# Kernel optimization log

Measured on AMD Instinct MI355X. Metric: run time of the kernel, lower is better.

## Reference

```python
import jax, jax.numpy as jnp
import numpy as np

TOP_K = 8
ALPHA = 0.1
EPS = 1e-20


def setup_inputs() -> dict:
    key = jax.random.key(0)
    k1, k2 = jax.random.split(key)
    B, S, D, E = 4, 8192, 1024, 64
    hidden_states = jax.random.normal(k1, (B, S, D), dtype=jnp.float32)
    # kaiming_uniform_(a=sqrt(5)) on [E, D] -> bound = 1/sqrt(D)
    bound = 1.0 / np.sqrt(D)
    W = jax.random.uniform(k2, (E, D), dtype=jnp.float32, minval=-bound, maxval=bound)
    return {"hidden_states": hidden_states, "W": W}


def reference(hidden_states, W):
    B, S, D = hidden_states.shape
    E = W.shape[0]
    x = hidden_states.reshape(-1, D)                       # [T, D], T = B*S
    logits = jnp.einsum('td,ed->te', x, W)                 # [T, E]
    scores = jax.nn.softmax(logits, axis=-1)               # [T, E]
    top_k_weights, top_k_idx = jax.lax.top_k(scores, TOP_K)  # [T, K]
    # norm_topk_experts renormalization
    top_k_weights = top_k_weights / (top_k_weights.sum(axis=-1, keepdims=True) + EPS)
    # seq_aux loss: per-batch expert selection counts via scatter-add
    idx = top_k_idx.reshape(B, -1)                         # [B, S*K]
    ce = jnp.zeros((B, E), dtype=jnp.float32).at[jnp.arange(B)[:, None], idx].add(1.0)
    mean_scores = scores.reshape(B, S, E).mean(axis=1)     # [B, E]
    aux_loss = (ce * mean_scores).sum(axis=1).mean() * ALPHA
    return top_k_idx, top_k_weights, aux_loss
```

## Files before the change

### kernel.cpp

```cpp
#include <hip/hip_runtime.h>

#define TOKS   32768
#define NEXP   64
#define DDIM   1024
#define SEQ    8192
#define NBATCH 4
#define TPB    64
#define STR    68
#define CSTR   21
#define BK     128
#define NCHK   (DDIM / BK)

typedef __attribute__((ext_vector_type(8)))  short short8v;
typedef __attribute__((ext_vector_type(16))) float f32x16;

__device__ __forceinline__ unsigned f2bf(float x) {
  unsigned u = __float_as_uint(x);
  return (u + 0x7fffu + ((u >> 16) & 1u)) >> 16;
}
__device__ __forceinline__ float bf2f(unsigned h) { return __uint_as_float(h << 16); }

__global__ void moe_wsplit(const float* __restrict__ W, ushort* __restrict__ W3) {
  const int sid = blockIdx.x * 256 + threadIdx.x;
  const int p  = sid & 3;
  const int e  = (sid >> 2) & 63;
  const int g  = sid >> 8;
  const int kh = p & 1;
  const int k0 = g * 16 + kh * 8;
  const float* src = W + (size_t)e * DDIM + k0;
  float f[8];
  *(float4*)&f[0] = *(const float4*)src;
  *(float4*)&f[4] = *(const float4*)(src + 4);
  ushort o[8];
  if (p < 2) {
#pragma unroll
    for (int j = 0; j < 8; ++j) o[j] = (ushort)f2bf(f[j]);
  } else {
#pragma unroll
    for (int j = 0; j < 8; ++j) {
      unsigned hb = f2bf(f[j]);
      o[j] = (ushort)f2bf(f[j] - bf2f(hb));
    }
  }
  *(short8v*)(W3 + (size_t)sid * 8) = *(const short8v*)o;
}

__global__ __launch_bounds__(256, 3) void moe_gate_main(
    const float* __restrict__ X, const ushort* __restrict__ W3,
    float* __restrict__ out, float* __restrict__ gsum, float* __restrict__ gce,
    int* __restrict__ flag_cnt, int* __restrict__ flag_tok)
{
  __shared__ __align__(16) char smem[47104];

  float* xs   = (float*)smem;
  float* wsm  = (float*)(smem + 17408);
  float* red  = (float*)(smem + 34816);
  float* gmx  = (float*)(smem + 35840);
  float* cval = (float*)(smem + 36096);
  int*   cidx = (int*)  (smem + 41472);
  int*   hist = (int*)  (smem + 46848);

  const int tid = threadIdx.x;
  const int tok_base = blockIdx.x * TPB;
  const int bb = blockIdx.x >> 7;

  const int l = tid & 63, q = tid >> 6;
  const int wm = q >> 1, wn = q & 1;
  const int rr = l & 31;
  const int kh = l >> 5;

  const int xr0 = tid >> 5;
  const int xc  = tid & 31;
  const float* Xbase = X + (size_t)tok_base * DDIM;
  int wb[8];
#pragma unroll
  for (int i = 0; i < 8; ++i) {
    const int r = xr0 + 8 * i;
    wb[i] = r * 256 + ((((xc >> 1) ^ (r & 15)) << 4)) + ((xc & 1) * 8);
  }

  const int abase = (wm * 32 + rr) * 256;
  const int amask = (wm * 32 + rr) & 15;
  const ushort* Wb = W3 + (size_t)(wn * 32 + rr) * 32 + kh * 8;

  f32x16 accA = (f32x16)0.0f, accB = (f32x16)0.0f;

  float4 px[8];
  unsigned sh[16], sl[16];

#define LOADPX(kc) do { \
    const float* xsrc = Xbase + (kc) * BK; \
    _Pragma("unroll") \
    for (int i = 0; i < 8; ++i) \
      px[i] = *(const float4*)(xsrc + (size_t)(xr0 + 8 * i) * DDIM + xc * 4); \
  } while (0)

#define CONV() do { \
    _Pragma("unroll") \
    for (int i = 0; i < 8; ++i) { \
      unsigned h0 = f2bf(px[i].x), h1 = f2bf(px[i].y); \
      unsigned h2 = f2bf(px[i].z), h3 = f2bf(px[i].w); \
      sh[2 * i]     = h0 | (h1 << 16); \
      sh[2 * i + 1] = h2 | (h3 << 16); \
      sl[2 * i]     = f2bf(px[i].x - bf2f(h0)) | (f2bf(px[i].y - bf2f(h1)) << 16); \
      sl[2 * i + 1] = f2bf(px[i].z - bf2f(h2)) | (f2bf(px[i].w - bf2f(h3)) << 16); \
    } } while (0)

#define WRITE() do { \
    _Pragma("unroll") \
    for (int i = 0; i < 8; ++i) { \
      *(uint2*)(smem + wb[i])         = make_uint2(sh[2 * i], sh[2 * i + 1]); \
      *(uint2*)(smem + 16384 + wb[i]) = make_uint2(sl[2 * i], sl[2 * i + 1]); \
    } } while (0)

#define COMPUTE(kc) do { \
    _Pragma("unroll") \
    for (int s = 0; s < 8; ++s) { \
      const int g = (kc) * 8 + s; \
      const ushort* wp = Wb + (size_t)g * 2048; \
      short8v bh = *(const short8v*)wp; \
      short8v bl = *(const short8v*)(wp + 16); \
      const int aoff = abase + (((2 * s + kh) ^ amask) << 4); \
      short8v ah = *(const short8v*)(smem + aoff); \
      short8v al = *(const short8v*)(smem + 16384 + aoff); \
      accA = __builtin_amdgcn_mfma_f32_32x32x16_bf16(ah, bh, accA, 0, 0, 0); \
      accB = __builtin_amdgcn_mfma_f32_32x32x16_bf16(al, bh, accB, 0, 0, 0); \
      accA = __builtin_amdgcn_mfma_f32_32x32x16_bf16(ah, bl, accA, 0, 0, 0); \
    } } while (0)

  LOADPX(0);
  CONV();
  WRITE();
  __syncthreads();

#pragma unroll 1
  for (int kc = 0; kc < NCHK; ++kc) {
    if (kc + 1 < NCHK) LOADPX(kc + 1);
    COMPUTE(kc);
    if (kc + 1 < NCHK) CONV();
    __syncthreads();
    if (kc + 1 < NCHK) {
      WRITE();
      __syncthreads();
    }
  }

  {
    const int ccol = wn * 32 + rr;
#pragma unroll
    for (int r = 0; r < 16; ++r) {
      const int trow = wm * 32 + (r & 3) + 8 * (r >> 2) + 4 * kh;
      wsm[trow * STR + ccol] = accA[r] + accB[r];
    }
  }
  if (tid < 64) hist[tid] = 0;
  __syncthreads();

#undef LOADPX
#undef CONV
#undef WRITE
#undef COMPUTE

  float* logits  = wsm;
  float* scoresT = xs;
  const int t = l;

  float m = -__builtin_huge_valf();
#pragma unroll
  for (int e = 0; e < 16; ++e) m = fmaxf(m, logits[t * STR + q * 16 + e]);
  red[q * 64 + t] = m;
  __syncthreads();
  float gm = fmaxf(fmaxf(red[t], red[64 + t]), fmaxf(red[128 + t], red[192 + t]));
  if (q == 0) gmx[t] = gm;
  float z = 0.0f;
#pragma unroll
  for (int e = 0; e < 16; ++e) {
    float ev = expf(logits[t * STR + q * 16 + e] - gm);
    scoresT[(q * 16 + e) * STR + t] = ev;
    z += ev;
  }
  __syncthreads();
  red[q * 64 + t] = z;
  __syncthreads();
  float Z = red[t] + red[64 + t] + red[128 + t] + red[192 + t];
  float invZ = 1.0f / Z;
#pragma unroll
  for (int e = 0; e < 16; ++e) scoresT[(q * 16 + e) * STR + t] *= invZ;
  __syncthreads();

  {
    const int e = l, g = q;
    float s = 0.0f;
#pragma unroll
    for (int tt = 0; tt < 16; ++tt) s += scoresT[e * STR + g * 16 + tt];
    red[g * 64 + e] = s;
  }
  __syncthreads();
  if (tid < 64) {
    float tot = red[tid] + red[64 + tid] + red[128 + tid] + red[192 + tid];
    atomicAdd(&gsum[bb * 64 + tid], tot);
  }

  if (tid < 128) {
    const int h = tid >> 6;
    const int eb = h * 32;
#pragma unroll 1
    for (int k = 0; k < 9; ++k) {
      float mv = -1.0f; int mi = eb;
#pragma unroll 4
      for (int e = 0; e < 32; ++e) {
        float v = scoresT[(eb + e) * STR + t];
        if (v > mv) { mv = v; mi = eb + e; }
      }
      cval[t * CSTR + h * 9 + k] = mv;
      cidx[t * CSTR + h * 9 + k] = mi;
      scoresT[mi * STR + t] = -1.0f;
    }
  }
  __syncthreads();

  if (tid < 64) {
    float wv[9]; int wi[8];
#pragma unroll 1
    for (int k = 0; k < 9; ++k) {
      float mv = -1.0f; int mj = 0;
#pragma unroll 3
      for (int j = 0; j < 18; ++j) {
        float v = cval[t * CSTR + j];
        if (v > mv) { mv = v; mj = j; }
      }
      wv[k] = mv;
      if (k < 8) {
        wi[k] = cidx[t * CSTR + mj];
        atomicAdd(&hist[wi[k]], 1);
      }
      cval[t * CSTR + mj] = -1.0f;
    }
    bool flag = false;
#pragma unroll
    for (int k = 0; k < 8; ++k)
      if (wv[k + 1] >= wv[k] * (1.0f - 2.0e-5f)) flag = true;
    if (flag) {
      int p = atomicAdd(flag_cnt, 1);
      flag_tok[p] = tok_base + t;
    }
    double ed[8]; double den = 0.0;
#pragma unroll
    for (int k = 0; k < 8; ++k) {
      ed[k] = exp((double)logits[t * STR + wi[k]] - (double)gmx[t]);
      den += ed[k];
    }
    const size_t tg = (size_t)(tok_base + t);
    *(float4*)(out + tg * 8) =
        make_float4((float)wi[0], (float)wi[1], (float)wi[2], (float)wi[3]);
    *(float4*)(out + tg * 8 + 4) =
        make_float4((float)wi[4], (float)wi[5], (float)wi[6], (float)wi[7]);
    *(float4*)(out + (size_t)TOKS * 8 + tg * 8) =
        make_float4((float)(ed[0] / den), (float)(ed[1] / den),
                    (float)(ed[2] / den), (float)(ed[3] / den));
    *(float4*)(out + (size_t)TOKS * 8 + tg * 8 + 4) =
        make_float4((float)(ed[4] / den), (float)(ed[5] / den),
                    (float)(ed[6] / den), (float)(ed[7] / den));
  }
  __syncthreads();
  if (tid < 64) atomicAdd(&gce[bb * 64 + tid], (float)hist[tid]);
}

__global__ __launch_bounds__(256) void moe_refine(
    const float* __restrict__ X, const float* __restrict__ W,
    float* __restrict__ out, float* __restrict__ gce,
    const int* __restrict__ flag_cnt, const int* __restrict__ flag_tok)
{
  __shared__ __align__(16) float xrow[DDIM];
  __shared__ double part[4][NEXP];
  const int tid = threadIdx.x;
  const int n = *flag_cnt;
  const int e = tid & 63;
  const int c = tid >> 6;
#pragma unroll 1
  for (int it = blockIdx.x; it < n; it += 256) {
    const int tok = flag_tok[it];
    __syncthreads();
    *(float4*)&xrow[tid * 4] = *(const float4*)&X[(size_t)tok * DDIM + tid * 4];
    __syncthreads();
    const float* wr = W + (size_t)e * DDIM + c * 256;
    const float* xr = xrow + c * 256;
    double s0 = 0.0, s1 = 0.0, s2 = 0.0, s3 = 0.0;
#pragma unroll 4
    for (int j = 0; j < 256; j += 4) {
      s0 += (double)xr[j]     * (double)wr[j];
      s1 += (double)xr[j + 1] * (double)wr[j + 1];
      s2 += (double)xr[j + 2] * (double)wr[j + 2];
      s3 += (double)xr[j + 3] * (double)wr[j + 3];
    }
    part[c][e] = (s0 + s1) + (s2 + s3);
    __syncthreads();
    if (tid < 64) {
      double cur = (part[0][e] + part[1][e]) + (part[2][e] + part[3][e]);
      int wi[8]; double wl[8];
#pragma unroll 1
      for (int k = 0; k < 8; ++k) {
        double mv = cur; int mi = e;
#pragma unroll
        for (int off = 1; off < 64; off <<= 1) {
          double ov = __shfl_xor(mv, off);
          int    oi = __shfl_xor(mi, off);
          if (ov > mv || (ov == mv && oi < mi)) { mv = ov; mi = oi; }
        }
        wi[k] = mi; wl[k] = mv;
        if (e == mi) cur = -1.0e300;
      }
      if (e == 0) {
        int olde[8];
#pragma unroll
        for (int k = 0; k < 8; ++k) olde[k] = (int)out[(size_t)tok * 8 + k];
        double ex[8]; double den = 0.0;
#pragma unroll
        for (int k = 0; k < 8; ++k) { ex[k] = exp(wl[k] - wl[0]); den += ex[k]; }
#pragma unroll
        for (int k = 0; k < 8; ++k) {
          out[(size_t)tok * 8 + k] = (float)wi[k];
          out[(size_t)TOKS * 8 + (size_t)tok * 8 + k] = (float)(ex[k] / den);
        }
        const int bbb = tok >> 13;
#pragma unroll 1
        for (int k = 0; k < 8; ++k) {
          bool in_new = false, in_old = false;
          for (int j = 0; j < 8; ++j) {
            if (wi[j] == olde[k]) in_new = true;
            if (olde[j] == wi[k]) in_old = true;
          }
          if (!in_new) atomicAdd(&gce[bbb * 64 + olde[k]], -1.0f);
          if (!in_old) atomicAdd(&gce[bbb * 64 + wi[k]], 1.0f);
        }
      }
    }
  }
}

__global__ void moe_gate_aux(const float* __restrict__ gsum,
                             const float* __restrict__ gce,
                             float* __restrict__ out)
{
  __shared__ float r[256];
  const int tid = threadIdx.x;
  r[tid] = gce[tid] * gsum[tid];
  __syncthreads();
  for (int s = 128; s > 0; s >>= 1) {
    if (tid < s) r[tid] += r[tid + s];
    __syncthreads();
  }
  if (tid == 0)
    out[(size_t)TOKS * 16] = 0.1f * r[0] / ((float)SEQ * (float)NBATCH);
}

extern "C" void kernel_launch(void* const* d_in, const int* in_sizes, int n_in,
                              void* d_out, int out_size, void* d_ws, size_t ws_size,
                              hipStream_t stream)
{
  const float* X = (const float*)d_in[0];
  const float* W = (const float*)d_in[1];
  float* out  = (float*)d_out;
  float* gsum = (float*)d_ws;
  float* gce  = gsum + NBATCH * NEXP;
  int* flag_cnt = (int*)((char*)d_ws + 2048);
  int* flag_tok = (int*)((char*)d_ws + 2176);
  ushort* W3 = (ushort*)((char*)d_ws + (1 << 20));

  hipMemsetAsync(d_ws, 0, 2176, stream);
  moe_wsplit<<<64, 256, 0, stream>>>(W, W3);
  moe_gate_main<<<TOKS / TPB, 256, 0, stream>>>(X, W3, out, gsum, gce, flag_cnt, flag_tok);
  moe_refine<<<256, 256, 0, stream>>>(X, W, out, gce, flag_cnt, flag_tok);
  moe_gate_aux<<<1, 256, 0, stream>>>(gsum, gce, out);
}
```

Baseline: 254.9 us.

## Split gate GEMM into separate small-tile kernel with double-buffered LDS

The fused GEMM and softmax/top-k kernel is split in two. A new GEMM kernel handles 16 tokens per block with 16x16x32 MFMAs, a double-buffered LDS tile, and one __syncthreads per K chunk, and it writes fp32 logits to workspace. A separate epilogue kernel reads those logits back and does softmax/top-k. The aim is more blocks, higher occupancy and better latency hiding for the memory-bound X stream, paid for with an extra logits round trip through global memory and one more launch.

```diff
diff --git a/kernel.cpp b/kernel.cpp
--- a/kernel.cpp
+++ b/kernel.cpp
@@ -8,11 +8,9 @@
 #define TPB    64
 #define STR    68
 #define CSTR   21
-#define BK     128
-#define NCHK   (DDIM / BK)
 
 typedef __attribute__((ext_vector_type(8)))  short short8v;
-typedef __attribute__((ext_vector_type(16))) float f32x16;
+typedef __attribute__((ext_vector_type(4)))  float f32x4;
 
 __device__ __forceinline__ unsigned f2bf(float x) {
   unsigned u = __float_as_uint(x);
@@ -20,19 +18,21 @@
 }
 __device__ __forceinline__ float bf2f(unsigned h) { return __uint_as_float(h << 16); }
 
-__global__ void moe_wsplit(const float* __restrict__ W, ushort* __restrict__ W3) {
+__global__ void moe_wsplit(const float* __restrict__ W, ushort* __restrict__ W4) {
   const int sid = blockIdx.x * 256 + threadIdx.x;
-  const int p  = sid & 3;
-  const int e  = (sid >> 2) & 63;
-  const int g  = sid >> 8;
-  const int kh = p & 1;
-  const int k0 = g * 16 + kh * 8;
+  const int table = sid >> 13;
+  const int s2 = sid & 8191;
+  const int g  = s2 >> 8;
+  const int r  = s2 & 255;
+  const int e  = r >> 2;
+  const int kh = r & 3;
+  const int k0 = g * 32 + kh * 8;
   const float* src = W + (size_t)e * DDIM + k0;
   float f[8];
   *(float4*)&f[0] = *(const float4*)src;
   *(float4*)&f[4] = *(const float4*)(src + 4);
   ushort o[8];
-  if (p < 2) {
+  if (table == 0) {
 #pragma unroll
     for (int j = 0; j < 8; ++j) o[j] = (ushort)f2bf(f[j]);
   } else {
@@ -42,11 +42,97 @@
       o[j] = (ushort)f2bf(f[j] - bf2f(hb));
     }
   }
-  *(short8v*)(W3 + (size_t)sid * 8) = *(const short8v*)o;
-}
-
-__global__ __launch_bounds__(256, 3) void moe_gate_main(
-    const float* __restrict__ X, const ushort* __restrict__ W3,
+  *(short8v*)(W4 + (size_t)sid * 8) = *(const short8v*)o;
+}
+
+__global__ __launch_bounds__(256, 6) void moe_gemm(
+    const float* __restrict__ X, const ushort* __restrict__ W4,
+    float* __restrict__ Lg)
+{
+  __shared__ __align__(16) char smem[16384];
+
+  const int tid = threadIdx.x;
+  const int l = tid & 63, w = tid >> 6;
+  const int tok_base = blockIdx.x * 16;
+
+  const int sr = tid >> 4;
+  const int sp = tid & 15;
+  const float* Xr = X + (size_t)(tok_base + sr) * DDIM + sp * 8;
+  const int wofs = sr * 256 + ((sp ^ sr) << 4);
+
+  const int kg = l >> 4;
+  const int abase = (l & 15) * 256;
+  const int axor = l & 15;
+  const char* Wb = (const char*)W4 + w * 1024 + (l & 15) * 64 + kg * 16;
+
+  f32x4 acc = (f32x4)0.0f;
+  float4 px0, px1;
+  unsigned vh[4], vl[4];
+
+#define LOADPX(kc) do { \
+    px0 = *(const float4*)(Xr + (kc) * 128); \
+    px1 = *(const float4*)(Xr + (kc) * 128 + 4); } while (0)
+
+#define CONV() do { \
+    float ff[8] = {px0.x, px0.y, px0.z, px0.w, px1.x, px1.y, px1.z, px1.w}; \
+    _Pragma("unroll") \
+    for (int i = 0; i < 4; ++i) { \
+      unsigned h0 = f2bf(ff[2 * i]), h1 = f2bf(ff[2 * i + 1]); \
+      vh[i] = h0 | (h1 << 16); \
+      vl[i] = f2bf(ff[2 * i] - bf2f(h0)) | (f2bf(ff[2 * i + 1] - bf2f(h1)) << 16); \
+    } } while (0)
+
+#define WRITE(b) do { \
+    *(uint4*)(smem + (b) * 8192 + wofs)        = make_uint4(vh[0], vh[1], vh[2], vh[3]); \
+    *(uint4*)(smem + (b) * 8192 + 4096 + wofs) = make_uint4(vl[0], vl[1], vl[2], vl[3]); \
+    } while (0)
+
+#define COMPUTE(kc) do { \
+    const char* base = smem + ((kc) & 1) * 8192; \
+    _Pragma("unroll") \
+    for (int s = 0; s < 4; ++s) { \
+      const char* wp = Wb + (size_t)((kc) * 4 + s) * 4096; \
+      short8v bh = *(const short8v*)wp; \
+      short8v bl = *(const short8v*)(wp + 131072); \
+      const int aoff = abase + (((4 * s + kg) ^ axor) << 4); \
+      short8v ah = *(const short8v*)(base + aoff); \
+      short8v al = *(const short8v*)(base + aoff + 4096); \
+      acc = __builtin_amdgcn_mfma_f32_16x16x32_bf16(ah, bh, acc, 0, 0, 0); \
+      acc = __builtin_amdgcn_mfma_f32_16x16x32_bf16(al, bh, acc, 0, 0, 0); \
+      acc = __builtin_amdgcn_mfma_f32_16x16x32_bf16(ah, bl, acc, 0, 0, 0); \
+    } } while (0)
+
+  LOADPX(0);
+  CONV();
+  WRITE(0);
+  LOADPX(1);
+  __syncthreads();
+
+#pragma unroll 1
+  for (int kc = 0; kc < 8; ++kc) {
+    if (kc + 1 < 8) {
+      CONV();
+      WRITE((kc + 1) & 1);
+    }
+    if (kc + 2 < 8) LOADPX(kc + 2);
+    COMPUTE(kc);
+    __syncthreads();
+  }
+
+#undef LOADPX
+#undef CONV
+#undef WRITE
+#undef COMPUTE
+
+  {
+    float* dst = Lg + (size_t)(tok_base + kg * 4) * NEXP + w * 16 + (l & 15);
+#pragma unroll
+    for (int r = 0; r < 4; ++r) dst[(size_t)r * NEXP] = acc[r];
+  }
+}
+
+__global__ __launch_bounds__(256, 3) void moe_gate_epi(
+    const float* __restrict__ Lg,
     float* __restrict__ out, float* __restrict__ gsum, float* __restrict__ gce,
     int* __restrict__ flag_cnt, int* __restrict__ flag_tok)
 {
@@ -63,103 +149,17 @@
   const int tid = threadIdx.x;
   const int tok_base = blockIdx.x * TPB;
   const int bb = blockIdx.x >> 7;
-
   const int l = tid & 63, q = tid >> 6;
-  const int wm = q >> 1, wn = q & 1;
-  const int rr = l & 31;
-  const int kh = l >> 5;
-
-  const int xr0 = tid >> 5;
-  const int xc  = tid & 31;
-  const float* Xbase = X + (size_t)tok_base * DDIM;
-  int wb[8];
-#pragma unroll
-  for (int i = 0; i < 8; ++i) {
-    const int r = xr0 + 8 * i;
-    wb[i] = r * 256 + ((((xc >> 1) ^ (r & 15)) << 4)) + ((xc & 1) * 8);
-  }
-
-  const int abase = (wm * 32 + rr) * 256;
-  const int amask = (wm * 32 + rr) & 15;
-  const ushort* Wb = W3 + (size_t)(wn * 32 + rr) * 32 + kh * 8;
-
-  f32x16 accA = (f32x16)0.0f, accB = (f32x16)0.0f;
-
-  float4 px[8];
-  unsigned sh[16], sl[16];
-
-#define LOADPX(kc) do { \
-    const float* xsrc = Xbase + (kc) * BK; \
-    _Pragma("unroll") \
-    for (int i = 0; i < 8; ++i) \
-      px[i] = *(const float4*)(xsrc + (size_t)(xr0 + 8 * i) * DDIM + xc * 4); \
-  } while (0)
-
-#define CONV() do { \
-    _Pragma("unroll") \
-    for (int i = 0; i < 8; ++i) { \
-      unsigned h0 = f2bf(px[i].x), h1 = f2bf(px[i].y); \
-      unsigned h2 = f2bf(px[i].z), h3 = f2bf(px[i].w); \
-      sh[2 * i]     = h0 | (h1 << 16); \
-      sh[2 * i + 1] = h2 | (h3 << 16); \
-      sl[2 * i]     = f2bf(px[i].x - bf2f(h0)) | (f2bf(px[i].y - bf2f(h1)) << 16); \
-      sl[2 * i + 1] = f2bf(px[i].z - bf2f(h2)) | (f2bf(px[i].w - bf2f(h3)) << 16); \
-    } } while (0)
-
-#define WRITE() do { \
-    _Pragma("unroll") \
-    for (int i = 0; i < 8; ++i) { \
-      *(uint2*)(smem + wb[i])         = make_uint2(sh[2 * i], sh[2 * i + 1]); \
-      *(uint2*)(smem + 16384 + wb[i]) = make_uint2(sl[2 * i], sl[2 * i + 1]); \
-    } } while (0)
-
-#define COMPUTE(kc) do { \
-    _Pragma("unroll") \
-    for (int s = 0; s < 8; ++s) { \
-      const int g = (kc) * 8 + s; \
-      const ushort* wp = Wb + (size_t)g * 2048; \
-      short8v bh = *(const short8v*)wp; \
-      short8v bl = *(const short8v*)(wp + 16); \
-      const int aoff = abase + (((2 * s + kh) ^ amask) << 4); \
-      short8v ah = *(const short8v*)(smem + aoff); \
-      short8v al = *(const short8v*)(smem + 16384 + aoff); \
-      accA = __builtin_amdgcn_mfma_f32_32x32x16_bf16(ah, bh, accA, 0, 0, 0); \
-      accB = __builtin_amdgcn_mfma_f32_32x32x16_bf16(al, bh, accB, 0, 0, 0); \
-      accA = __builtin_amdgcn_mfma_f32_32x32x16_bf16(ah, bl, accA, 0, 0, 0); \
-    } } while (0)
-
-  LOADPX(0);
-  CONV();
-  WRITE();
-  __syncthreads();
-
-#pragma unroll 1
-  for (int kc = 0; kc < NCHK; ++kc) {
-    if (kc + 1 < NCHK) LOADPX(kc + 1);
-    COMPUTE(kc);
-    if (kc + 1 < NCHK) CONV();
-    __syncthreads();
-    if (kc + 1 < NCHK) {
-      WRITE();
-      __syncthreads();
-    }
-  }
-
-  {
-    const int ccol = wn * 32 + rr;
-#pragma unroll
-    for (int r = 0; r < 16; ++r) {
-      const int trow = wm * 32 + (r & 3) + 8 * (r >> 2) + 4 * kh;
-      wsm[trow * STR + ccol] = accA[r] + accB[r];
-    }
+
+  const float* Ls = Lg + (size_t)tok_base * NEXP;
+#pragma unroll
+  for (int i = 0; i < 4; ++i) {
+    const int id = i * 256 + tid;
+    float4 v = *(const float4*)(Ls + id * 4);
+    *(float4*)&wsm[(id >> 4) * STR + (id & 15) * 4] = v;
   }
   if (tid < 64) hist[tid] = 0;
   __syncthreads();
-
-#undef LOADPX
-#undef CONV
-#undef WRITE
-#undef COMPUTE
 
   float* logits  = wsm;
   float* scoresT = xs;
@@ -365,11 +365,13 @@
   float* gce  = gsum + NBATCH * NEXP;
   int* flag_cnt = (int*)((char*)d_ws + 2048);
   int* flag_tok = (int*)((char*)d_ws + 2176);
-  ushort* W3 = (ushort*)((char*)d_ws + (1 << 20));
+  ushort* W4 = (ushort*)((char*)d_ws + (1 << 20));
+  float*  Lg = (float*)((char*)d_ws + (2 << 20));
 
   hipMemsetAsync(d_ws, 0, 2176, stream);
-  moe_wsplit<<<64, 256, 0, stream>>>(W, W3);
-  moe_gate_main<<<TOKS / TPB, 256, 0, stream>>>(X, W3, out, gsum, gce, flag_cnt, flag_tok);
+  moe_wsplit<<<64, 256, 0, stream>>>(W, W4);
+  moe_gemm<<<TOKS / 16, 256, 0, stream>>>(X, W4, Lg);
+  moe_gate_epi<<<TOKS / TPB, 256, 0, stream>>>(Lg, out, gsum, gce, flag_cnt, flag_tok);
   moe_refine<<<256, 256, 0, stream>>>(X, W, out, gce, flag_cnt, flag_tok);
   moe_gate_aux<<<1, 256, 0, stream>>>(gsum, gce, out);
 }
```

Measured after the change: 253.8 us. No clear change (-0.4%).
